# Kernel tuning notes

Measured on AMD Instinct MI355X. Metric: run time of the kernel, lower is better.

The kernel has to match this reference:

```python
import jax, jax.numpy as jnp
import numpy as np

B, L, HEADS, D_HEAD = 2, 2048, 16, 64
D_MODEL = HEADS * D_HEAD            # 1024
D_BI = D_MODEL * 4 // 2             # 2048 (bilinear GLU width)
D_PROJ = D_MODEL * 3 + 2 * D_BI
DEPTH = 0                           # block depth < 2 -> token shift active
NEG_INF = -1e10


def _ln(x, g, b, eps=1e-5):
    m = jnp.mean(x, axis=-1, keepdims=True)
    v = jnp.var(x, axis=-1, keepdims=True)
    return (x - m) * jax.lax.rsqrt(v + eps) * g + b


def _shift(x, n):
    # F.pad(x, (0,0,n,-n)): shift along seq dim by n, zero-fill at front
    return jnp.pad(x, ((0, 0), (n, 0), (0, 0)))[:, : x.shape[1], :]


def setup_inputs() -> dict:
    key = jax.random.key(0)
    ks = jax.random.split(key, 3)
    x = jax.random.normal(ks[0], (B, L, D_MODEL), jnp.float32)
    w_in = jax.random.normal(ks[1], (D_MODEL, D_PROJ), jnp.float32) * (D_MODEL ** -0.5)
    # note: torch init zeros out_proj; we use small random weights so backward is non-trivial
    w_out = jax.random.normal(ks[2], (D_MODEL + D_BI, D_MODEL), jnp.float32) * 0.02
    slopes = jnp.concatenate([2.0 ** jnp.linspace(0.0, -6.0, HEADS // 2),
                              jnp.zeros(HEADS - HEADS // 2)]).astype(jnp.float32)
    return {
        "x": x,
        "in_ln_g": jnp.ones(D_MODEL, jnp.float32), "in_ln_b": jnp.zeros(D_MODEL, jnp.float32),
        "mid_ln_g": jnp.ones(D_PROJ, jnp.float32), "mid_ln_b": jnp.zeros(D_PROJ, jnp.float32),
        "out_ln_g": jnp.ones(D_MODEL, jnp.float32), "out_ln_b": jnp.zeros(D_MODEL, jnp.float32),
        "w_in": w_in, "w_out": w_out, "slopes": slopes,
    }


def reference(x, in_ln_g, in_ln_b, mid_ln_g, mid_ln_b, out_ln_g, out_ln_b, w_in, w_out, slopes):
    b, l, d = x.shape
    x = _ln(x, in_ln_g, in_ln_b)
    if DEPTH < 2:
        x = jnp.concatenate([
            _shift(x[..., : d // 4], 1),
            x[..., d // 4: d - d // 8],
            _shift(x[..., d - d // 8:], 2),
        ], axis=-1)
    h = _ln(x @ w_in, mid_ln_g, mid_ln_b)
    q, k, v, p1, p2 = jnp.split(h, [D_MODEL, 2 * D_MODEL, 3 * D_MODEL, 3 * D_MODEL + D_BI], axis=-1)
    to_heads = lambda t: t.reshape(b, l, HEADS, D_HEAD).transpose(0, 2, 1, 3)  # b h l d
    q, k, v = to_heads(q), to_heads(k), to_heads(v)
    logits = jnp.einsum('bhid,bhjd->bhij', q, k) * (D_HEAD ** -0.5)
    pos = jnp.arange(l)
    alibi = pos[None, None, None, :].astype(logits.dtype) * slopes[None, :, None, None]
    causal = jnp.where(pos[:, None] >= pos[None, :], 0.0, NEG_INF).astype(logits.dtype)
    a = jax.nn.softmax(logits + alibi + causal, axis=-1)
    o = jnp.einsum('bhij,bhjd->bhid', a, v).transpose(0, 2, 1, 3).reshape(b, l, d)
    return _ln(jnp.concatenate([o, p1 * p2], axis=-1) @ w_out, out_ln_g, out_ln_b)
```

## Files before the change

kernel.cpp:

```cpp
#include <hip/hip_runtime.h>

#define B_ 2
#define L_ 2048
#define HEADS_ 16
#define DH_ 64
#define DM_ 1024
#define DBI_ 2048
#define DPROJ_ 7168
#define NTOK (B_*L_)
#define DCAT (DM_ + DBI_)

typedef __bf16 bf16;
typedef __attribute__((ext_vector_type(8))) __bf16 bf16x8;
typedef __attribute__((ext_vector_type(4))) __bf16 bf16x4;
typedef __attribute__((ext_vector_type(4))) float floatx4;

typedef __attribute__((address_space(1))) const void gptr_t;
typedef __attribute__((address_space(3))) void lptr_t;

__device__ __forceinline__ void g2l16(const void* g, void* l) {
    __builtin_amdgcn_global_load_lds((gptr_t*)g, (lptr_t*)l, 16, 0, 0);
}

__global__ __launch_bounds__(256) void transpose_both(const float* __restrict__ w_in,
                                                      const float* __restrict__ w_out,
                                                      bf16* __restrict__ w_inT,
                                                      bf16* __restrict__ w_outT) {
    __shared__ float tile[32][33];
    int l = blockIdx.x;
    const float* in; bf16* outp; int R, C, bx, by;
    if (l < 7168) { in = w_in;  outp = w_inT;  R = DM_;  C = DPROJ_; bx = l % 224; by = l / 224; }
    else { l -= 7168; in = w_out; outp = w_outT; R = DCAT; C = DM_;   bx = l % 32;  by = l / 32; }
    int c0 = bx * 32, r0 = by * 32;
    int x = threadIdx.x & 31, y = threadIdx.x >> 5;
    for (int i = 0; i < 32; i += 8)
        tile[y + i][x] = in[(size_t)(r0 + y + i) * C + (c0 + x)];
    __syncthreads();
    for (int i = 0; i < 32; i += 8)
        outp[(size_t)(c0 + y + i) * R + (r0 + x)] = (bf16)tile[x][y + i];
}

__global__ __launch_bounds__(256) void ln_shift(const float* __restrict__ x,
                                                const float* __restrict__ g,
                                                const float* __restrict__ bb,
                                                bf16* __restrict__ xs) {
    int tok = blockIdx.x;
    int b = tok / L_, l = tok % L_;
    int t = threadIdx.x;
    floatx4 v = *(const floatx4*)(x + (size_t)tok * DM_ + t * 4);
    float s = v[0] + v[1] + v[2] + v[3];
    float s2 = v[0]*v[0] + v[1]*v[1] + v[2]*v[2] + v[3]*v[3];
    __shared__ float red[2][4];
    for (int o = 32; o; o >>= 1) { s += __shfl_xor(s, o); s2 += __shfl_xor(s2, o); }
    int w = t >> 6;
    if ((t & 63) == 0) { red[0][w] = s; red[1][w] = s2; }
    __syncthreads();
    s  = red[0][0] + red[0][1] + red[0][2] + red[0][3];
    s2 = red[1][0] + red[1][1] + red[1][2] + red[1][3];
    float mean = s * (1.f / DM_);
    float var  = s2 * (1.f / DM_) - mean * mean;
    float rstd = rsqrtf(var + 1e-5f);
    int c0 = t * 4;
    floatx4 gg = *(const floatx4*)(g + c0);
    floatx4 bv = *(const floatx4*)(bb + c0);
    bf16x4 y;
    #pragma unroll
    for (int i = 0; i < 4; i++) y[i] = (bf16)((v[i] - mean) * rstd * gg[i] + bv[i]);
    int shift = (c0 < 256) ? 1 : ((c0 >= 896) ? 2 : 0);
    int dl = l + shift;
    if (dl < L_) *(bf16x4*)(xs + ((size_t)b * L_ + dl) * DM_ + c0) = y;
    if (l == 0 && shift) {
        bf16x4 z = {};
        *(bf16x4*)(xs + ((size_t)b * L_ + 0) * DM_ + c0) = z;
        if (shift == 2) *(bf16x4*)(xs + ((size_t)b * L_ + 1) * DM_ + c0) = z;
    }
}

__global__ __launch_bounds__(512, 2) void gemm1_fr(const bf16* __restrict__ A,
                                                   const bf16* __restrict__ Bt,
                                                   bf16* __restrict__ C) {
    const int K = DM_, N = DPROJ_;
    int lin = blockIdx.x;
    int xcd = lin & 7, idx = lin >> 3;
    int mt = (xcd >> 2) * 8 + idx / 7;
    int nt = (xcd & 3) * 7 + idx % 7;
    int m0 = mt * 256, n0 = nt * 256;

    __shared__ bf16 As[2][256 * 64];
    __shared__ bf16 Bs[2][256 * 64];

    int t = threadIdx.x;
    int lane = t & 63;
    int c = lane & 15, quad = lane >> 4;
    int wave = t >> 6;
    int wm = (wave >> 2) * 128;
    int wn = (wave & 3) * 64;

    auto stageA = [&](int k0, int bsel, int h) {
        #pragma unroll
        for (int s = 0; s < 2; s++) {
            int g = h * 1024 + s * 512 + t;
            int row = g >> 3;
            int kc = (g & 7) ^ (row & 7);
            g2l16(A + (size_t)(m0 + row) * K + (k0 + kc * 8), &As[bsel][g * 8]);
        }
    };
    auto stageB = [&](int k0, int bsel, int h) {
        #pragma unroll
        for (int s = 0; s < 2; s++) {
            int g = h * 1024 + s * 512 + t;
            int row = g >> 3;
            int kc = (g & 7) ^ (row & 7);
            g2l16(Bt + (size_t)(n0 + row) * K + (k0 + kc * 8), &Bs[bsel][g * 8]);
        }
    };

    floatx4 acc[8][4] = {};

    stageA(0, 0, 0); stageA(0, 0, 1);
    stageB(0, 0, 0); stageB(0, 0, 1);
    stageB(64, 1, 0); stageB(64, 1, 1);
    asm volatile("s_waitcnt vmcnt(4)" ::: "memory");
    __builtin_amdgcn_s_barrier();
    __builtin_amdgcn_sched_barrier(0);

    const int nT = K / 64;
    for (int tt = 0; tt < nT; ++tt) {
        int cur = tt & 1, nxt = cur ^ 1;
        int k1 = (tt + 1) << 6, k2 = (tt + 2) << 6;
        bool dA = (tt + 1 < nT), dB = (tt + 2 < nT);
        bf16x8 bfr[4][2];
        #pragma unroll
        for (int p = 0; p < 4; p++) {
            if      (p == 0) { if (dA) stageA(k1, nxt, 0); }
            else if (p == 1) { if (dA) stageA(k1, nxt, 1); }
            else if (p == 2) { if (dB) stageB(k2, cur, 0); }
            else             { if (dB) stageB(k2, cur, 1); }
            if (p == 0) {
                #pragma unroll
                for (int j = 0; j < 4; j++)
                    #pragma unroll
                    for (int s = 0; s < 2; s++)
                        bfr[j][s] = *(const bf16x8*)&Bs[cur][(wn + j * 16 + c) * 64
                                                            + (((s * 4 + quad) ^ (c & 7)) * 8)];
            }
            bf16x8 af[2][2];
            #pragma unroll
            for (int ii = 0; ii < 2; ii++)
                #pragma unroll
                for (int s = 0; s < 2; s++)
                    af[ii][s] = *(const bf16x8*)&As[cur][(wm + (p * 2 + ii) * 16 + c) * 64
                                                         + (((s * 4 + quad) ^ (c & 7)) * 8)];
            __builtin_amdgcn_s_setprio(1);
            #pragma unroll
            for (int ii = 0; ii < 2; ii++)
                #pragma unroll
                for (int j = 0; j < 4; j++)
                    #pragma unroll
                    for (int s = 0; s < 2; s++)
                        acc[p * 2 + ii][j] = __builtin_amdgcn_mfma_f32_16x16x32_bf16(
                            af[ii][s], bfr[j][s], acc[p * 2 + ii][j], 0, 0, 0);
            __builtin_amdgcn_s_setprio(0);
        }
        asm volatile("s_waitcnt lgkmcnt(0)" ::: "memory");
        if (dB)      { asm volatile("s_waitcnt vmcnt(4)" ::: "memory"); }
        else if (dA) { asm volatile("s_waitcnt vmcnt(0)" ::: "memory"); }
        if (tt + 1 < nT) __builtin_amdgcn_s_barrier();
        __builtin_amdgcn_sched_barrier(0);
    }

    #pragma unroll
    for (int i = 0; i < 8; i++)
        #pragma unroll
        for (int j = 0; j < 4; j++)
            #pragma unroll
            for (int r = 0; r < 4; r++) {
                int row = m0 + wm + i * 16 + quad * 4 + r;
                int col = n0 + wn + j * 16 + c;
                C[(size_t)row * N + col] = (bf16)acc[i][j][r];
            }
}

__global__ __launch_bounds__(256, 2) void gemm2_fr(const bf16* __restrict__ A,
                                                   const bf16* __restrict__ Bt,
                                                   float* __restrict__ P) {
    const int ldA = DCAT, N = DM_;
    int m0 = blockIdx.x * 128, n0 = blockIdx.y * 128, kz = blockIdx.z;
    const bf16* Ak = A + kz * 1536;
    const bf16* Btk = Bt + kz * 1536;
    float* C = P + (size_t)kz * NTOK * DM_;
    __shared__ bf16 As[2][128 * 64];
    __shared__ bf16 Bs[2][128 * 64];
    int t = threadIdx.x, lane = t & 63, wave = t >> 6;
    int c = lane & 15, quad = lane >> 4;
    int wm = (wave >> 1) * 64, wn = (wave & 1) * 64;

    auto stageA = [&](int k0, int bsel, int h) {
        #pragma unroll
        for (int s = 0; s < 2; s++) {
            int g = h * 512 + s * 256 + t;
            int row = g >> 3;
            int kc = (g & 7) ^ (row & 7);
            g2l16(Ak + (size_t)(m0 + row) * ldA + k0 + kc * 8, &As[bsel][g * 8]);
        }
    };
    auto stageB = [&](int k0, int bsel, int h) {
        #pragma unroll
        for (int s = 0; s < 2; s++) {
            int g = h * 512 + s * 256 + t;
            int row = g >> 3;
            int kc = (g & 7) ^ (row & 7);
            g2l16(Btk + (size_t)(n0 + row) * ldA + k0 + kc * 8, &Bs[bsel][g * 8]);
        }
    };

    floatx4 acc[4][4] = {};

    stageA(0, 0, 0); stageA(0, 0, 1);
    stageB(0, 0, 0); stageB(0, 0, 1);
    stageB(64, 1, 0); stageB(64, 1, 1);
    asm volatile("s_waitcnt vmcnt(4)" ::: "memory");
    __builtin_amdgcn_s_barrier();
    __builtin_amdgcn_sched_barrier(0);

    const int nT = 1536 / 64;
    for (int tt = 0; tt < nT; ++tt) {
        int cur = tt & 1, nxt = cur ^ 1;
        int k1 = (tt + 1) << 6, k2 = (tt + 2) << 6;
        bool dA = (tt + 1 < nT), dB = (tt + 2 < nT);
        bf16x8 bfr[4][2];
        #pragma unroll
        for (int p = 0; p < 4; p++) {
            if      (p == 0) { if (dA) stageA(k1, nxt, 0); }
            else if (p == 1) { if (dA) stageA(k1, nxt, 1); }
            else if (p == 2) { if (dB) stageB(k2, cur, 0); }
            else             { if (dB) stageB(k2, cur, 1); }
            if (p == 0) {
                #pragma unroll
                for (int j = 0; j < 4; j++)
                    #pragma unroll
                    for (int s = 0; s < 2; s++)
                        bfr[j][s] = *(const bf16x8*)&Bs[cur][(wn + j * 16 + c) * 64
                                                            + (((s * 4 + quad) ^ (c & 7)) * 8)];
            }
            bf16x8 af[2];
            #pragma unroll
            for (int s = 0; s < 2; s++)
                af[s] = *(const bf16x8*)&As[cur][(wm + p * 16 + c) * 64
                                                 + (((s * 4 + quad) ^ (c & 7)) * 8)];
            __builtin_amdgcn_s_setprio(1);
            #pragma unroll
            for (int j = 0; j < 4; j++)
                #pragma unroll
                for (int s = 0; s < 2; s++)
                    acc[p][j] = __builtin_amdgcn_mfma_f32_16x16x32_bf16(
                        af[s], bfr[j][s], acc[p][j], 0, 0, 0);
            __builtin_amdgcn_s_setprio(0);
        }
        asm volatile("s_waitcnt lgkmcnt(0)" ::: "memory");
        if (dB)      { asm volatile("s_waitcnt vmcnt(4)" ::: "memory"); }
        else if (dA) { asm volatile("s_waitcnt vmcnt(0)" ::: "memory"); }
        if (tt + 1 < nT) __builtin_amdgcn_s_barrier();
        __builtin_amdgcn_sched_barrier(0);
    }

    #pragma unroll
    for (int p = 0; p < 4; p++)
        #pragma unroll
        for (int j = 0; j < 4; j++)
            #pragma unroll
            for (int r = 0; r < 4; r++) {
                int row = m0 + wm + p * 16 + quad * 4 + r;
                int col = n0 + wn + j * 16 + c;
                C[(size_t)row * N + col] = acc[p][j][r];
            }
}

__global__ __launch_bounds__(448) void mid_ln_fused(const bf16* __restrict__ h,
                                                    const float* __restrict__ g,
                                                    const float* __restrict__ bb,
                                                    bf16* __restrict__ Qp,
                                                    bf16* __restrict__ Kp,
                                                    bf16* __restrict__ Vn,
                                                    bf16* __restrict__ A2) {
    int tok = blockIdx.x;
    int b = tok >> 11, l = tok & 2047;
    size_t base = (size_t)tok * DPROJ_;
    int t = threadIdx.x;
    int c0, c1;
    if (t < 256) { c0 = 384 + t; c1 = 640 + t; }
    else { int u = t - 256; c0 = 2 * u; c1 = 2 * u + 1; }
    bf16x8 r0 = *(const bf16x8*)(h + base + c0 * 8);
    bf16x8 r1 = *(const bf16x8*)(h + base + c1 * 8);
    float v0[8], v1[8];
    float s = 0.f, s2 = 0.f;
    #pragma unroll
    for (int i = 0; i < 8; i++) {
        v0[i] = (float)r0[i]; v1[i] = (float)r1[i];
        s += v0[i] + v1[i]; s2 += v0[i] * v0[i] + v1[i] * v1[i];
    }
    __shared__ float red[2][7];
    for (int o = 32; o; o >>= 1) { s += __shfl_xor(s, o); s2 += __shfl_xor(s2, o); }
    int w = t >> 6;
    if ((t & 63) == 0) { red[0][w] = s; red[1][w] = s2; }
    __syncthreads();
    s = 0.f; s2 = 0.f;
    #pragma unroll
    for (int i = 0; i < 7; i++) { s += red[0][i]; s2 += red[1][i]; }
    float mean = s * (1.f / DPROJ_);
    float var  = s2 * (1.f / DPROJ_) - mean * mean;
    float rstd = rsqrtf(var + 1e-5f);
    floatx4 g0a = *(const floatx4*)(g + c0 * 8),  g0b = *(const floatx4*)(g + c0 * 8 + 4);
    floatx4 b0a = *(const floatx4*)(bb + c0 * 8), b0b = *(const floatx4*)(bb + c0 * 8 + 4);
    floatx4 g1a = *(const floatx4*)(g + c1 * 8),  g1b = *(const floatx4*)(g + c1 * 8 + 4);
    floatx4 b1a = *(const floatx4*)(bb + c1 * 8), b1b = *(const floatx4*)(bb + c1 * 8 + 4);
    float y0[8], y1[8];
    #pragma unroll
    for (int i = 0; i < 4; i++) {
        y0[i]     = (v0[i]     - mean) * rstd * g0a[i] + b0a[i];
        y0[i + 4] = (v0[i + 4] - mean) * rstd * g0b[i] + b0b[i];
        y1[i]     = (v1[i]     - mean) * rstd * g1a[i] + b1a[i];
        y1[i + 4] = (v1[i + 4] - mean) * rstd * g1b[i] + b1b[i];
    }
    if (t < 256) {
        bf16x8 pv;
        #pragma unroll
        for (int i = 0; i < 8; i++) pv[i] = (bf16)(y0[i] * y1[i]);
        *(bf16x8*)(A2 + (size_t)tok * DCAT + DM_ + t * 8) = pv;
    } else {
        auto wchunk = [&](int c8, float* y) {
            int C0 = c8 * 8;
            int sec = C0 >> 10, cc = C0 & 1023;
            int hh = cc >> 6, d = cc & 63;
            size_t idx = (((size_t)b * HEADS_ + hh) * L_ + l) * DH_ + d;
            bf16* dst = (sec == 0) ? Qp : (sec == 1) ? Kp : Vn;
            bf16x8 o;
            #pragma unroll
            for (int i = 0; i < 8; i++) o[i] = (bf16)y[i];
            *(bf16x8*)(dst + idx) = o;
        };
        wchunk(c0, y0);
        wchunk(c1, y1);
    }
}

__global__ __launch_bounds__(256) void vt_pack(const bf16* __restrict__ Vn,
                                               bf16* __restrict__ Vt) {
    __shared__ bf16 tile[32][33];
    int bh = blockIdx.z;
    const bf16* in = Vn + (size_t)bh * L_ * DH_;
    bf16* out = Vt + (size_t)bh * DH_ * L_;
    int l0 = blockIdx.x * 32, d0 = blockIdx.y * 32;
    int x = threadIdx.x & 31, y = threadIdx.x >> 5;
    for (int i = 0; i < 32; i += 8)
        tile[y + i][x] = in[(size_t)(l0 + y + i) * DH_ + d0 + x];
    __syncthreads();
    for (int i = 0; i < 32; i += 8)
        out[(size_t)(d0 + y + i) * L_ + l0 + x] = tile[x][y + i];
}

__global__ __launch_bounds__(256, 4) void attn6(const bf16* __restrict__ Qp,
                                                const bf16* __restrict__ Kp,
                                                const bf16* __restrict__ Vt,
                                                const float* __restrict__ slopes,
                                                bf16* __restrict__ A2) {
    int hd = blockIdx.y, b = blockIdx.z;
    int lin = blockIdx.x + 32 * blockIdx.y + 512 * blockIdx.z;
    int xr = blockIdx.x;
    int qt = ((lin >> 8) & 1) ? (31 - xr) : xr;
    int q0 = qt * 64;
    int t = threadIdx.x, lane = t & 63, wave = t >> 6;
    int quad = lane >> 4, c = lane & 15;
    __shared__ bf16 Ks[2][64 * 64];
    __shared__ bf16 Vs[64 * 64];
    __shared__ bf16 Ps[4][16 * 72];
    int bh = b * HEADS_ + hd;
    const bf16* Qb = Qp + (size_t)bh * L_ * DH_;
    const bf16* Kb = Kp + (size_t)bh * L_ * DH_;
    const bf16* Vb = Vt + (size_t)bh * DH_ * L_;
    const float LOG2E = 1.44269504f;
    float slopeL2 = slopes[hd] * LOG2E;
    const float qscale = 0.125f * LOG2E;

    bf16x8 qf[2];
    int qrow = q0 + wave * 16 + c;
    qf[0] = *(const bf16x8*)(Qb + (size_t)qrow * DH_ + quad * 8);
    qf[1] = *(const bf16x8*)(Qb + (size_t)qrow * DH_ + 32 + quad * 8);
    floatx4 accO[4] = {};
    float lsum[4];
    float mrow[4];
    int i_row0 = q0 + wave * 16 + quad * 4;
    #pragma unroll
    for (int r = 0; r < 4; r++) {
        lsum[r] = 0.f;
        mrow[r] = slopeL2 * (float)(i_row0 + r) + 20.0f;
    }

    int row = t >> 2, kp = (t & 3) * 8;
    auto stageK = [&](int j0, int kb) {
        #pragma unroll
        for (int s = 0; s < 2; s++)
            g2l16(Kb + (size_t)(j0 + row) * DH_ + s * 32 + kp, &Ks[kb][(s * 256 + t) * 8]);
    };
    auto stageV = [&](int j0) {
        #pragma unroll
        for (int s = 0; s < 2; s++)
            g2l16(Vb + (size_t)row * L_ + j0 + s * 32 + kp, &Vs[(s * 256 + t) * 8]);
    };

    bf16* pw = &Ps[wave][0];
    bf16* pwr = pw + (quad * 4) * 72 + c;

    stageK(0, 0);
    asm volatile("s_waitcnt vmcnt(0)" ::: "memory");
    __builtin_amdgcn_s_barrier();
    __builtin_amdgcn_sched_barrier(0);

    int kb = 0;
    for (int j0 = 0; j0 <= q0; j0 += 64) {
        bool dK = (j0 + 64 <= q0);
        stageV(j0);
        if (dK) stageK(j0 + 64, kb ^ 1);

        bool diag = (j0 == q0);
        #pragma unroll
        for (int nt = 0; nt < 4; nt++) {
            floatx4 sacc = {};
            bf16x8 kf0 = *(const bf16x8*)&Ks[kb][(nt * 16 + c) * 32 + quad * 8];
            bf16x8 kf1 = *(const bf16x8*)&Ks[kb][2048 + (nt * 16 + c) * 32 + quad * 8];
            sacc = __builtin_amdgcn_mfma_f32_16x16x32_bf16(qf[0], kf0, sacc, 0, 0, 0);
            sacc = __builtin_amdgcn_mfma_f32_16x16x32_bf16(qf[1], kf1, sacc, 0, 0, 0);
            int j = j0 + nt * 16 + c;
            float aj = slopeL2 * (float)j;
            #pragma unroll
            for (int r = 0; r < 4; r++) {
                float p = exp2f(fmaf(sacc[r], qscale, aj) - mrow[r]);
                if (diag) p = (j <= i_row0 + r) ? p : 0.f;
                lsum[r] += p;
                pwr[r * 72 + nt * 16] = (bf16)p;
            }
        }
        bf16x8 pf0 = *(const bf16x8*)&pw[c * 72 + quad * 8];
        bf16x8 pf1 = *(const bf16x8*)&pw[c * 72 + 32 + quad * 8];

        if (dK) { asm volatile("s_waitcnt vmcnt(2)" ::: "memory"); }
        else    { asm volatile("s_waitcnt vmcnt(0)" ::: "memory"); }
        __builtin_amdgcn_s_barrier();
        __builtin_amdgcn_sched_barrier(0);

        #pragma unroll
        for (int nt = 0; nt < 4; nt++) {
            bf16x8 vf0 = *(const bf16x8*)&Vs[(nt * 16 + c) * 32 + quad * 8];
            bf16x8 vf1 = *(const bf16x8*)&Vs[2048 + (nt * 16 + c) * 32 + quad * 8];
            accO[nt] = __builtin_amdgcn_mfma_f32_16x16x32_bf16(pf0, vf0, accO[nt], 0, 0, 0);
            accO[nt] = __builtin_amdgcn_mfma_f32_16x16x32_bf16(pf1, vf1, accO[nt], 0, 0, 0);
        }
        asm volatile("s_waitcnt lgkmcnt(0)" ::: "memory");
        __builtin_amdgcn_s_barrier();
        __builtin_amdgcn_sched_barrier(0);
        kb ^= 1;
    }
    #pragma unroll
    for (int r = 0; r < 4; r++) {
        float l = lsum[r];
        l += __shfl_xor(l, 1);
        l += __shfl_xor(l, 2);
        l += __shfl_xor(l, 4);
        l += __shfl_xor(l, 8);
        lsum[r] = 1.f / l;
    }
    #pragma unroll
    for (int r = 0; r < 4; r++) {
        size_t orow = (size_t)b * L_ + q0 + wave * 16 + quad * 4 + r;
        #pragma unroll
        for (int nt = 0; nt < 4; nt++)
            A2[orow * DCAT + hd * DH_ + nt * 16 + c] = (bf16)(accO[nt][r] * lsum[r]);
    }
}

__global__ __launch_bounds__(256) void out_ln2(const float* __restrict__ P,
                                               const float* __restrict__ g,
                                               const float* __restrict__ bb,
                                               float* __restrict__ out) {
    size_t base = (size_t)blockIdx.x * DM_;
    const size_t stride = (size_t)NTOK * DM_;
    int t = threadIdx.x;
    floatx4 a = *(const floatx4*)(P + base + t * 4);
    floatx4 b4 = *(const floatx4*)(P + base + stride + t * 4);
    floatx4 v;
    #pragma unroll
    for (int i = 0; i < 4; i++) v[i] = a[i] + b4[i];
    float s = v[0] + v[1] + v[2] + v[3];
    float s2 = v[0]*v[0] + v[1]*v[1] + v[2]*v[2] + v[3]*v[3];
    __shared__ float red[2][4];
    for (int o = 32; o; o >>= 1) { s += __shfl_xor(s, o); s2 += __shfl_xor(s2, o); }
    int w = t >> 6;
    if ((t & 63) == 0) { red[0][w] = s; red[1][w] = s2; }
    __syncthreads();
    s  = red[0][0] + red[0][1] + red[0][2] + red[0][3];
    s2 = red[1][0] + red[1][1] + red[1][2] + red[1][3];
    float mean = s * (1.f / DM_);
    float var  = s2 * (1.f / DM_) - mean * mean;
    float rstd = rsqrtf(var + 1e-5f);
    int c0 = t * 4;
    floatx4 gg = *(const floatx4*)(g + c0);
    floatx4 bv = *(const floatx4*)(bb + c0);
    floatx4 o;
    #pragma unroll
    for (int i = 0; i < 4; i++) o[i] = (v[i] - mean) * rstd * gg[i] + bv[i];
    *(floatx4*)(out + base + c0) = o;
}

extern "C" void kernel_launch(void* const* d_in, const int* in_sizes, int n_in,
                              void* d_out, int out_size, void* d_ws, size_t ws_size,
                              hipStream_t stream) {
    const float* x     = (const float*)d_in[0];
    const float* in_g  = (const float*)d_in[1];
    const float* in_b  = (const float*)d_in[2];
    const float* mid_g = (const float*)d_in[3];
    const float* mid_b = (const float*)d_in[4];
    const float* out_g = (const float*)d_in[5];
    const float* out_b = (const float*)d_in[6];
    const float* w_in  = (const float*)d_in[7];
    const float* w_out = (const float*)d_in[8];
    const float* slopes = (const float*)d_in[9];
    float* out = (float*)d_out;

    char* ws = (char*)d_ws;
    size_t off = 0;
    auto alloc = [&](size_t n) { char* p = ws + off; off += (n + 255) & ~(size_t)255; return p; };
    bf16* w_inT  = (bf16*)alloc((size_t)DPROJ_ * DM_ * 2);
    bf16* w_outT = (bf16*)alloc((size_t)DM_ * DCAT * 2);
    bf16* xs     = (bf16*)alloc((size_t)NTOK * DM_ * 2);
    bf16* h      = (bf16*)alloc((size_t)NTOK * DPROJ_ * 2);
    bf16* A2     = (bf16*)alloc((size_t)NTOK * DCAT * 2);
    bf16* Qp     = (bf16*)alloc((size_t)NTOK * DM_ * 2);
    bf16* Kp     = (bf16*)alloc((size_t)NTOK * DM_ * 2);
    bf16* Vn     = (bf16*)alloc((size_t)NTOK * DM_ * 2);
    bf16* Vt = xs;
    float* P = (float*)h;

    hipLaunchKernelGGL(transpose_both, dim3(7168 + 3072), dim3(256), 0, stream,
                       w_in, w_out, w_inT, w_outT);
    hipLaunchKernelGGL(ln_shift, dim3(NTOK), dim3(256), 0, stream, x, in_g, in_b, xs);
    hipLaunchKernelGGL(gemm1_fr, dim3(448), dim3(512), 0, stream, xs, w_inT, h);
    hipLaunchKernelGGL(mid_ln_fused, dim3(NTOK), dim3(448), 0, stream, h, mid_g, mid_b,
                       Qp, Kp, Vn, A2);
    hipLaunchKernelGGL(vt_pack, dim3(L_ / 32, DH_ / 32, B_ * HEADS_), dim3(256), 0, stream, Vn, Vt);
    hipLaunchKernelGGL(attn6, dim3(32, HEADS_, B_), dim3(256), 0, stream, Qp, Kp, Vt, slopes, A2);
    hipLaunchKernelGGL(gemm2_fr, dim3(NTOK / 128, DM_ / 128, 2), dim3(256), 0, stream,
                       A2, w_outT, P);
    hipLaunchKernelGGL(out_ln2, dim3(NTOK), dim3(256), 0, stream, P, out_g, out_b, out);
}
```

Baseline: 335.9 us.

## Raise output GEMM split-K to three with simpler double-buffered kernel

Replaces the tuned output-projection GEMM with a split-K-3 kernel. It uses a 32-wide K tile, plain double buffering with one block barrier per step, and no LDS swizzle. The final layernorm kernel now sums three partial buffers instead of two. The aim is more blocks in flight across the GPU, at the cost of an extra fp32 partial buffer to write and read back. It also gives up the hand-tuned staggered load and priority scheduling and risks LDS bank conflicts.

```diff
diff --git a/kernel.cpp b/kernel.cpp
--- a/kernel.cpp
+++ b/kernel.cpp
@@ -181,98 +181,57 @@
             }
 }
 
-__global__ __launch_bounds__(256, 2) void gemm2_fr(const bf16* __restrict__ A,
-                                                   const bf16* __restrict__ Bt,
-                                                   float* __restrict__ P) {
+__global__ __launch_bounds__(256) void gemm2_sk(const bf16* __restrict__ A,
+                                                const bf16* __restrict__ Bt,
+                                                float* __restrict__ P) {
     const int ldA = DCAT, N = DM_;
     int m0 = blockIdx.x * 128, n0 = blockIdx.y * 128, kz = blockIdx.z;
-    const bf16* Ak = A + kz * 1536;
-    const bf16* Btk = Bt + kz * 1536;
+    const bf16* Ak = A + kz * 1024;
+    const bf16* Btk = Bt + kz * 1024;
     float* C = P + (size_t)kz * NTOK * DM_;
-    __shared__ bf16 As[2][128 * 64];
-    __shared__ bf16 Bs[2][128 * 64];
+    __shared__ bf16 As[2][128 * 32];
+    __shared__ bf16 Bs[2][128 * 32];
     int t = threadIdx.x, lane = t & 63, wave = t >> 6;
     int c = lane & 15, quad = lane >> 4;
     int wm = (wave >> 1) * 64, wn = (wave & 1) * 64;
-
-    auto stageA = [&](int k0, int bsel, int h) {
+    auto stage = [&](int k0, int bsel) {
         #pragma unroll
         for (int s = 0; s < 2; s++) {
-            int g = h * 512 + s * 256 + t;
-            int row = g >> 3;
-            int kc = (g & 7) ^ (row & 7);
-            g2l16(Ak + (size_t)(m0 + row) * ldA + k0 + kc * 8, &As[bsel][g * 8]);
+            int f = s * 256 + t;
+            int row = f >> 2, kp = (f & 3) * 8;
+            g2l16(Ak + (size_t)(m0 + row) * ldA + k0 + kp, &As[bsel][f * 8]);
+            g2l16(Btk + (size_t)(n0 + row) * ldA + k0 + kp, &Bs[bsel][f * 8]);
         }
     };
-    auto stageB = [&](int k0, int bsel, int h) {
-        #pragma unroll
-        for (int s = 0; s < 2; s++) {
-            int g = h * 512 + s * 256 + t;
-            int row = g >> 3;
-            int kc = (g & 7) ^ (row & 7);
-            g2l16(Btk + (size_t)(n0 + row) * ldA + k0 + kc * 8, &Bs[bsel][g * 8]);
-        }
-    };
-
     floatx4 acc[4][4] = {};
-
-    stageA(0, 0, 0); stageA(0, 0, 1);
-    stageB(0, 0, 0); stageB(0, 0, 1);
-    stageB(64, 1, 0); stageB(64, 1, 1);
-    asm volatile("s_waitcnt vmcnt(4)" ::: "memory");
-    __builtin_amdgcn_s_barrier();
-    __builtin_amdgcn_sched_barrier(0);
-
-    const int nT = 1536 / 64;
-    for (int tt = 0; tt < nT; ++tt) {
-        int cur = tt & 1, nxt = cur ^ 1;
-        int k1 = (tt + 1) << 6, k2 = (tt + 2) << 6;
-        bool dA = (tt + 1 < nT), dB = (tt + 2 < nT);
-        bf16x8 bfr[4][2];
-        #pragma unroll
-        for (int p = 0; p < 4; p++) {
-            if      (p == 0) { if (dA) stageA(k1, nxt, 0); }
-            else if (p == 1) { if (dA) stageA(k1, nxt, 1); }
-            else if (p == 2) { if (dB) stageB(k2, cur, 0); }
-            else             { if (dB) stageB(k2, cur, 1); }
-            if (p == 0) {
-                #pragma unroll
-                for (int j = 0; j < 4; j++)
-                    #pragma unroll
-                    for (int s = 0; s < 2; s++)
-                        bfr[j][s] = *(const bf16x8*)&Bs[cur][(wn + j * 16 + c) * 64
-                                                            + (((s * 4 + quad) ^ (c & 7)) * 8)];
-            }
-            bf16x8 af[2];
-            #pragma unroll
-            for (int s = 0; s < 2; s++)
-                af[s] = *(const bf16x8*)&As[cur][(wm + p * 16 + c) * 64
-                                                 + (((s * 4 + quad) ^ (c & 7)) * 8)];
-            __builtin_amdgcn_s_setprio(1);
+    stage(0, 0);
+    int buf = 0;
+    for (int k0 = 0; k0 < 1024; k0 += 32) {
+        __syncthreads();
+        if (k0 + 32 < 1024) stage(k0 + 32, buf ^ 1);
+        bf16x8 af[4], bfr[4];
+        #pragma unroll
+        for (int i = 0; i < 4; i++)
+            af[i] = *(const bf16x8*)&As[buf][(wm + i * 16 + c) * 32 + quad * 8];
+        #pragma unroll
+        for (int j = 0; j < 4; j++)
+            bfr[j] = *(const bf16x8*)&Bs[buf][(wn + j * 16 + c) * 32 + quad * 8];
+        #pragma unroll
+        for (int i = 0; i < 4; i++)
             #pragma unroll
             for (int j = 0; j < 4; j++)
-                #pragma unroll
-                for (int s = 0; s < 2; s++)
-                    acc[p][j] = __builtin_amdgcn_mfma_f32_16x16x32_bf16(
-                        af[s], bfr[j][s], acc[p][j], 0, 0, 0);
-            __builtin_amdgcn_s_setprio(0);
-        }
-        asm volatile("s_waitcnt lgkmcnt(0)" ::: "memory");
-        if (dB)      { asm volatile("s_waitcnt vmcnt(4)" ::: "memory"); }
-        else if (dA) { asm volatile("s_waitcnt vmcnt(0)" ::: "memory"); }
-        if (tt + 1 < nT) __builtin_amdgcn_s_barrier();
-        __builtin_amdgcn_sched_barrier(0);
-    }
-
-    #pragma unroll
-    for (int p = 0; p < 4; p++)
+                acc[i][j] = __builtin_amdgcn_mfma_f32_16x16x32_bf16(af[i], bfr[j], acc[i][j], 0, 0, 0);
+        buf ^= 1;
+    }
+    #pragma unroll
+    for (int i = 0; i < 4; i++)
         #pragma unroll
         for (int j = 0; j < 4; j++)
             #pragma unroll
             for (int r = 0; r < 4; r++) {
-                int row = m0 + wm + p * 16 + quad * 4 + r;
+                int row = m0 + wm + i * 16 + quad * 4 + r;
                 int col = n0 + wn + j * 16 + c;
-                C[(size_t)row * N + col] = acc[p][j][r];
+                C[(size_t)row * N + col] = acc[i][j][r];
             }
 }
 
@@ -478,7 +437,7 @@
     }
 }
 
-__global__ __launch_bounds__(256) void out_ln2(const float* __restrict__ P,
+__global__ __launch_bounds__(256) void out_ln3(const float* __restrict__ P,
                                                const float* __restrict__ g,
                                                const float* __restrict__ bb,
                                                float* __restrict__ out) {
@@ -487,9 +446,10 @@
     int t = threadIdx.x;
     floatx4 a = *(const floatx4*)(P + base + t * 4);
     floatx4 b4 = *(const floatx4*)(P + base + stride + t * 4);
+    floatx4 c4 = *(const floatx4*)(P + base + 2 * stride + t * 4);
     floatx4 v;
     #pragma unroll
-    for (int i = 0; i < 4; i++) v[i] = a[i] + b4[i];
+    for (int i = 0; i < 4; i++) v[i] = a[i] + b4[i] + c4[i];
     float s = v[0] + v[1] + v[2] + v[3];
     float s2 = v[0]*v[0] + v[1]*v[1] + v[2]*v[2] + v[3]*v[3];
     __shared__ float red[2][4];
@@ -548,7 +508,7 @@
                        Qp, Kp, Vn, A2);
     hipLaunchKernelGGL(vt_pack, dim3(L_ / 32, DH_ / 32, B_ * HEADS_), dim3(256), 0, stream, Vn, Vt);
     hipLaunchKernelGGL(attn6, dim3(32, HEADS_, B_), dim3(256), 0, stream, Qp, Kp, Vt, slopes, A2);
-    hipLaunchKernelGGL(gemm2_fr, dim3(NTOK / 128, DM_ / 128, 2), dim3(256), 0, stream,
+    hipLaunchKernelGGL(gemm2_sk, dim3(NTOK / 128, DM_ / 128, 3), dim3(256), 0, stream,
                        A2, w_outT, P);
-    hipLaunchKernelGGL(out_ln2, dim3(NTOK), dim3(256), 0, stream, P, out_g, out_b, out);
-}
+    hipLaunchKernelGGL(out_ln3, dim3(NTOK), dim3(256), 0, stream, P, out_g, out_b, out);
+}
```

After: 322.0 us. -4.1%, faster.
